# Performance work log

Hardware: AMD Instinct MI355X
Metric: run time of the kernel (lower is better)

The kernel has to match this reference:

```python
import jax, jax.numpy as jnp
import numpy as np

D = 256      # d_v
FF = 512     # ff_dim = max(hidden, d_v)
H = 4        # num_heads
K = 8        # max_set_size
L = 64       # subset universe length
NC = 32768   # n_chains
NB = 4096    # n_batch
EPS = 1e-8   # module eps for masked-mean denom


def setup_inputs() -> dict:
    key = jax.random.key(0)
    ks = jax.random.split(key, 24)
    s = 0.02
    mask = jax.random.randint(ks[2], (NC, L), 0, 2).astype(bool)
    inp = {
        "v": jax.random.normal(ks[0], (NB, L, D), jnp.float32),
        "batch_idx": jax.random.randint(ks[1], (NC,), 0, NB),
        "mask": mask,
        "count": mask.sum(axis=1).astype(jnp.float32),
        "pos_embed": jnp.zeros((1, K, D), jnp.float32),
        "ln1_w": jnp.ones((D,), jnp.float32),
        "ln1_b": jnp.zeros((D,), jnp.float32),
        "in_proj_w": jax.random.normal(ks[3], (3 * D, D), jnp.float32) * s,
        "in_proj_b": jnp.zeros((3 * D,), jnp.float32),
        "out_proj_w": jax.random.normal(ks[4], (D, D), jnp.float32) * s,
        "out_proj_b": jnp.zeros((D,), jnp.float32),
        "ln2_w": jnp.ones((D,), jnp.float32),
        "ln2_b": jnp.zeros((D,), jnp.float32),
        "ff1_w": jax.random.normal(ks[5], (FF, D), jnp.float32) * s,
        "ff1_b": jnp.zeros((FF,), jnp.float32),
        "ff2_w": jax.random.normal(ks[6], (D, FF), jnp.float32) * s,
        "ff2_b": jnp.zeros((D,), jnp.float32),
        "o1_w": jax.random.normal(ks[7], (FF, D + 1), jnp.float32) * s,
        "o1_b": jnp.zeros((FF,), jnp.float32),
        "o2_w": jax.random.normal(ks[8], (D, FF), jnp.float32) * s,
        "o2_b": jnp.zeros((D,), jnp.float32),
    }
    return inp


def _layernorm(x, w, b, eps=1e-5):
    mu = x.mean(-1, keepdims=True)
    var = ((x - mu) ** 2).mean(-1, keepdims=True)
    return (x - mu) * jax.lax.rsqrt(var + eps) * w + b


def reference(v, batch_idx, mask, count, pos_embed, ln1_w, ln1_b, in_proj_w,
              in_proj_b, out_proj_w, out_proj_b, ln2_w, ln2_b, ff1_w, ff1_b,
              ff2_w, ff2_b, o1_w, o1_b, o2_w, o2_b):
    nc, Lm = mask.shape
    # --- topk subset select (index-order packing) ---
    pos = jnp.arange(Lm, dtype=jnp.float32)
    scores = mask.astype(jnp.float32) * (float(Lm) - pos)[None, :]
    top_scores, top_idx = jax.lax.top_k(scores, K)
    picked0 = top_scores > 0
    sortable = jnp.where(picked0, top_idx, Lm)
    sortable = jnp.sort(sortable, axis=1)
    picked = sortable < Lm                       # [NC,K]
    safe_idx = jnp.where(picked, sortable, 0)
    # fused gather: chain_v[c, i] = v[batch_idx[c], i]
    packed = v[batch_idx[:, None], safe_idx]     # [NC,K,D]
    packed = packed * picked[..., None].astype(packed.dtype)
    x = packed + pos_embed[:, :K, :]
    # key padding mask; un-mask position 0 for fully-empty sets
    kpm = ~picked
    empty = jnp.all(kpm, axis=1)
    kpm = kpm.at[:, 0].set(jnp.where(empty, False, kpm[:, 0]))
    # --- one pre-norm transformer encoder layer ---
    h = _layernorm(x, ln1_w, ln1_b)
    qkv = h @ in_proj_w.T + in_proj_b
    q, k_, vv = jnp.split(qkv, 3, axis=-1)
    hd = D // H
    def heads(t):
        return t.reshape(nc, K, H, hd).transpose(0, 2, 1, 3)
    q, k_, vv = heads(q), heads(k_), heads(vv)
    att = jnp.einsum('bhqd,bhkd->bhqk', q, k_) / jnp.sqrt(jnp.float32(hd))
    att = jnp.where(kpm[:, None, None, :], -jnp.inf, att)
    att = jax.nn.softmax(att, axis=-1)
    ao = jnp.einsum('bhqk,bhkd->bhqd', att, vv).transpose(0, 2, 1, 3).reshape(nc, K, D)
    x = x + ao @ out_proj_w.T + out_proj_b
    h2 = _layernorm(x, ln2_w, ln2_b)
    x = x + jax.nn.gelu(h2 @ ff1_w.T + ff1_b, approximate=False) @ ff2_w.T + ff2_b
    # --- masked mean pool ---
    pf = picked.astype(x.dtype)
    denom = jnp.maximum(pf.sum(axis=1, keepdims=True), EPS)
    pooled = (x * pf[..., None]).sum(axis=1) / denom
    pooled = jnp.where(picked.any(axis=1, keepdims=True), pooled, jnp.zeros_like(pooled))
    # --- concat log(1+|S|) and project ---
    feat = jnp.concatenate([pooled, jnp.log1p(count)[:, None]], axis=-1)
    return jax.nn.gelu(feat @ o1_w.T + o1_b, approximate=False) @ o2_w.T + o2_b
```

## Files before the change

### kernel.cpp

```cpp
#include <hip/hip_runtime.h>
#include <hip/hip_bf16.h>
#include <math.h>

typedef short short8 __attribute__((ext_vector_type(8)));
typedef short short4v __attribute__((ext_vector_type(4)));
typedef float f32x4 __attribute__((ext_vector_type(4)));

#define NCC  32768
#define G    4
#define QST  520

#define G1_OFF 0
#define G2_OFF 196608
#define G3_OFF 262144
#define G4_OFF 393216
#define O1_OFF 524288
#define O2_OFF 655360
#define SWZ_SHORTS 786432
#define W256_BYTE_OFF (SWZ_SHORTS * 2)
#define FLAG_BYTE_OFF (W256_BYTE_OFF + 2048)

__device__ __forceinline__ float gelu_f(float x) {
    return x * 0.5f * (1.0f + erff(x * 0.70710678118654752f));
}
__device__ __forceinline__ float bf2f(unsigned short u) {
    union { unsigned int i; float f; } w; w.i = ((unsigned int)u) << 16; return w.f;
}
__device__ __forceinline__ unsigned short f2bf(float f) {
    __hip_bfloat16 h = __float2bfloat16(f);
    return *reinterpret_cast<unsigned short*>(&h);
}
__device__ __forceinline__ int aswz(int row, int scol) {
    return (row * 256 + scol) ^ ((row & 7) << 3);
}
__device__ __forceinline__ int vtswz(int d, int j) {
    return d * 32 + (j ^ ((d & 7) << 2));
}

template<int KTS>
__device__ __forceinline__ void load_bgrp(short8 (&b)[KTS], const unsigned short* __restrict__ base) {
    #pragma unroll
    for (int kt = 0; kt < KTS; kt++)
        b[kt] = *reinterpret_cast<const short8*>(base + (size_t)kt * 512);
}

__global__ void conv_weights(const float* __restrict__ w1, const float* __restrict__ w2,
                             const float* __restrict__ w3, const float* __restrict__ w4,
                             const float* __restrict__ o1, const float* __restrict__ o2,
                             unsigned short* __restrict__ dst, float* __restrict__ w256) {
    int i = blockIdx.x * 256 + threadIdx.x;
    if (i < 98304) {
        const float* src; int kts, sk, base;
        if (i < 24576)      { src = w1; kts = 8;  sk = 256; base = 0; }
        else if (i < 32768) { src = w2; kts = 8;  sk = 256; base = 24576; }
        else if (i < 49152) { src = w3; kts = 8;  sk = 256; base = 32768; }
        else if (i < 65536) { src = w4; kts = 16; sk = 512; base = 49152; }
        else if (i < 81920) { src = o1; kts = 8;  sk = 257; base = 65536; }
        else                { src = o2; kts = 16; sk = 512; base = 81920; }
        int li   = i - base;
        int lane = li & 63;
        int fi   = li >> 6;
        int kt   = fi % kts;
        int nt   = fi / kts;
        int col  = nt * 16 + (lane & 15);
        int k    = kt * 32 + (lane >> 4) * 8;
        const float* s = src + (size_t)col * sk + k;
        unsigned short* d = dst + (size_t)i * 8;
        #pragma unroll
        for (int e = 0; e < 8; e++) d[e] = f2bf(s[e]);
    } else if (i < 98816) {
        int c = i - 98304;
        w256[c] = o1[(size_t)c * 257 + 256];
    }
}

__global__ void detect_mask_fmt(const unsigned int* __restrict__ mw, int nwords, int* __restrict__ flag) {
    __shared__ int s_bad_int, s_bad_float;
    if (threadIdx.x == 0) { s_bad_int = 0; s_bad_float = 0; }
    __syncthreads();
    int bad_int = 0, bad_float = 0;
    for (int i = threadIdx.x; i < nwords; i += blockDim.x) {
        unsigned int w = mw[i];
        if (w > 1u) bad_int = 1;
        if (w != 0u && w != 0x3F800000u) bad_float = 1;
    }
    if (bad_int)   atomicOr(&s_bad_int, 1);
    if (bad_float) atomicOr(&s_bad_float, 1);
    __syncthreads();
    if (threadIdx.x == 0)
        *flag = (!s_bad_int) ? 0 : ((!s_bad_float) ? 2 : 1);
}

__global__ __launch_bounds__(256, 2)
void tsa_main(const float* __restrict__ v,
              const int* __restrict__ batch_idx,
              const void* __restrict__ mask,
              const float* __restrict__ pos_embed,
              const float* __restrict__ ln1_w, const float* __restrict__ ln1_b,
              const float* __restrict__ in_proj_b,
              const float* __restrict__ out_proj_b,
              const float* __restrict__ ln2_w, const float* __restrict__ ln2_b,
              const float* __restrict__ ff1_b, const float* __restrict__ ff2_b,
              const unsigned short* __restrict__ wb,
              const int* __restrict__ mask_flag,
              float* __restrict__ out)
{
    __shared__ unsigned short qkbuf[32 * QST];
    __shared__ unsigned short abuf[32 * 256];
    __shared__ unsigned short attw_s[2][4][16][16];
    __shared__ int s_idx[G][8];
    __shared__ int s_m[G];
    __shared__ int s_bi[G];

    float (*lnred)[32][2] = reinterpret_cast<float (*)[32][2]>(&attw_s[0][0][0][0]);

    const int tid  = threadIdx.x;
    const int lane = tid & 63;
    const int wid  = tid >> 6;
    const int cq   = lane >> 4;
    const int cc   = lane & 15;
    const int cg0  = blockIdx.x * G;
    const int pair = wid >> 1;

    f32x4 xr[2][4];

    {
        int mf = *mask_flag;
        size_t base = (size_t)(cg0 + wid) * 64 + lane;
        int bit;
        if (mf == 0)      bit = ((const int*)mask)[base] != 0;
        else if (mf == 2) bit = ((const float*)mask)[base] != 0.0f;
        else              bit = ((const unsigned char*)mask)[base] != 0;
        unsigned long long bal = __ballot(bit);
        if (lane == 0) {
            int mm = 0; unsigned long long b = bal;
            while (b && mm < 8) { s_idx[wid][mm++] = __ffsll(b) - 1; b &= (b - 1); }
            for (int t = mm; t < 8; t++) s_idx[wid][t] = 0;
            s_m[wid]  = mm;
            s_bi[wid] = batch_idx[cg0 + wid];
        }
    }
    __syncthreads();

    #pragma unroll
    for (int mt = 0; mt < 2; mt++) {
        int c  = 2 * mt + (cq >> 1);
        int m  = s_m[c];
        int bi = s_bi[c];
        #pragma unroll
        for (int rr = 0; rr < 4; rr++) {
            int rowin = (cq & 1) * 4 + rr;
            int vidx  = s_idx[c][rowin];
            #pragma unroll
            for (int nt = 0; nt < 4; nt++) {
                int col  = wid * 64 + nt * 16 + cc;
                float pe = pos_embed[rowin * 256 + col];
                float val = (rowin < m) ? v[((size_t)bi * 64 + vidx) * 256 + col] : 0.0f;
                xr[mt][nt][rr] = val + pe;
            }
        }
    }

    auto do_ln = [&](const float* __restrict__ lw, const float* __restrict__ lb) {
        float sm[2][4], sq[2][4];
        #pragma unroll
        for (int mt = 0; mt < 2; mt++)
            #pragma unroll
            for (int rr = 0; rr < 4; rr++) {
                float s = 0.f, q = 0.f;
                #pragma unroll
                for (int nt = 0; nt < 4; nt++) {
                    float x = xr[mt][nt][rr];
                    s += x; q += x * x;
                }
                sm[mt][rr] = s; sq[mt][rr] = q;
            }
        #pragma unroll
        for (int off = 1; off < 16; off <<= 1) {
            #pragma unroll
            for (int mt = 0; mt < 2; mt++)
                #pragma unroll
                for (int rr = 0; rr < 4; rr++) {
                    sm[mt][rr] += __shfl_xor(sm[mt][rr], off);
                    sq[mt][rr] += __shfl_xor(sq[mt][rr], off);
                }
        }
        __syncthreads();
        if (cc == 0) {
            #pragma unroll
            for (int mt = 0; mt < 2; mt++)
                #pragma unroll
                for (int rr = 0; rr < 4; rr++) {
                    int row = mt * 16 + cq * 4 + rr;
                    lnred[wid][row][0] = sm[mt][rr];
                    lnred[wid][row][1] = sq[mt][rr];
                }
        }
        __syncthreads();
        float mu[2][4], rs[2][4];
        #pragma unroll
        for (int mt = 0; mt < 2; mt++)
            #pragma unroll
            for (int rr = 0; rr < 4; rr++) {
                int row = mt * 16 + cq * 4 + rr;
                float S = 0.f, Q = 0.f;
                #pragma unroll
                for (int w = 0; w < 4; w++) { S += lnred[w][row][0]; Q += lnred[w][row][1]; }
                float m_ = S * (1.0f / 256.0f);
                mu[mt][rr] = m_;
                rs[mt][rr] = rsqrtf(Q * (1.0f / 256.0f) - m_ * m_ + 1e-5f);
            }
        #pragma unroll
        for (int nt = 0; nt < 4; nt++) {
            int col = wid * 64 + nt * 16 + cc;
            float w_ = lw[col], b_ = lb[col];
            #pragma unroll
            for (int mt = 0; mt < 2; mt++)
                #pragma unroll
                for (int rr = 0; rr < 4; rr++) {
                    int row = mt * 16 + cq * 4 + rr;
                    abuf[aswz(row, col)] = f2bf((xr[mt][nt][rr] - mu[mt][rr]) * rs[mt][rr] * w_ + b_);
                }
        }
        __syncthreads();
    };

    auto load_a_from = [&](short8 (&a0)[8], short8 (&a1)[8], const unsigned short* base) {
        #pragma unroll
        for (int kt = 0; kt < 8; kt++) {
            a0[kt] = *reinterpret_cast<const short8*>(&base[aswz(cc,      kt * 32 + cq * 8)]);
            a1[kt] = *reinterpret_cast<const short8*>(&base[aswz(16 + cc, kt * 32 + cq * 8)]);
        }
    };

    do_ln(ln1_w, ln1_b);

    {
        short8 a0[8], a1[8];
        load_a_from(a0, a1, abuf);
        __syncthreads();

        auto bbase = [&](int nt) {
            int gnt = (nt < 8) ? (wid * 8 + nt) : (32 + wid * 4 + (nt - 8));
            return wb + G1_OFF + (size_t)gnt * 8 * 512 + lane * 8;
        };
        short8 bb[2][8];
        load_bgrp<8>(bb[0], bbase(0));
        #pragma unroll
        for (int nt = 0; nt < 12; nt++) {
            if (nt + 1 < 12) load_bgrp<8>(bb[(nt + 1) & 1], bbase(nt + 1));
            float b = (nt < 8) ? in_proj_b[wid * 128 + nt * 16 + cc]
                               : in_proj_b[512 + wid * 64 + (nt - 8) * 16 + cc];
            f32x4 c0 = {b, b, b, b}, c1 = {b, b, b, b};
            #pragma unroll
            for (int kt = 0; kt < 8; kt++) {
                c0 = __builtin_amdgcn_mfma_f32_16x16x32_bf16(a0[kt], bb[nt & 1][kt], c0, 0, 0, 0);
                c1 = __builtin_amdgcn_mfma_f32_16x16x32_bf16(a1[kt], bb[nt & 1][kt], c1, 0, 0, 0);
            }
            if (nt < 8) {
                int col = wid * 128 + nt * 16 + cc;
                #pragma unroll
                for (int r = 0; r < 4; r++) {
                    qkbuf[(cq * 4 + r) * QST + col]      = f2bf(c0[r]);
                    qkbuf[(16 + cq * 4 + r) * QST + col] = f2bf(c1[r]);
                }
            } else {
                int d = wid * 64 + (nt - 8) * 16 + cc;
                short4v p0, p1;
                #pragma unroll
                for (int r = 0; r < 4; r++) { p0[r] = (short)f2bf(c0[r]); p1[r] = (short)f2bf(c1[r]); }
                *reinterpret_cast<short4v*>(&abuf[vtswz(d, cq * 4)])      = p0;
                *reinterpret_cast<short4v*>(&abuf[vtswz(d, 16 + cq * 4)]) = p1;
            }
        }
    }
    __syncthreads();

    {
        #pragma unroll
        for (int hj = 0; hj < 2; hj++) {
            int h = (wid & 1) * 2 + hj;
            f32x4 c = {0.f, 0.f, 0.f, 0.f};
            #pragma unroll
            for (int kt = 0; kt < 2; kt++) {
                short8 qa = *reinterpret_cast<const short8*>(&qkbuf[(pair * 16 + cc) * QST + h * 64 + cq * 8 + kt * 32]);
                short8 kb = *reinterpret_cast<const short8*>(&qkbuf[(pair * 16 + cc) * QST + 256 + h * 64 + cq * 8 + kt * 32]);
                c = __builtin_amdgcn_mfma_f32_16x16x32_bf16(qa, kb, c, 0, 0, 0);
            }
            int jhalf = cc >> 3, jloc = cc & 7;
            #pragma unroll
            for (int r = 0; r < 4; r++) {
                int q = cq * 4 + r;
                int qhalf = q >> 3;
                int m = s_m[pair * 2 + qhalf];
                bool valid = (jhalf == qhalf) && (jloc < m);
                float s = valid ? c[r] * 0.125f : -1e30f;
                float mx = s;
                mx = fmaxf(mx, __shfl_xor(mx, 1));
                mx = fmaxf(mx, __shfl_xor(mx, 2));
                mx = fmaxf(mx, __shfl_xor(mx, 4));
                float e = valid ? __expf(s - mx) : 0.f;
                float se = e;
                se += __shfl_xor(se, 1);
                se += __shfl_xor(se, 2);
                se += __shfl_xor(se, 4);
                attw_s[pair][h][q][cc] = f2bf((se > 0.f) ? e / se : 0.f);
            }
        }
    }
    __syncthreads();

    {
        int jbg = pair * 16 + (cq & 1) * 8;
        #pragma unroll
        for (int hj = 0; hj < 2; hj++) {
            int h = (wid & 1) * 2 + hj;
            short8 pa;
            if (cq < 2) pa = *reinterpret_cast<const short8*>(&attw_s[pair][h][cc][cq * 8]);
            else        pa = (short8)((short)0);
            #pragma unroll
            for (int t = 0; t < 4; t++) {
                int d = h * 64 + t * 16 + cc;
                short4v lo = *reinterpret_cast<const short4v*>(&abuf[vtswz(d, jbg)]);
                short4v hi = *reinterpret_cast<const short4v*>(&abuf[vtswz(d, jbg + 4)]);
                union { short8 v; short4v half2[2]; } u;
                u.half2[0] = lo; u.half2[1] = hi;
                f32x4 c = {0.f, 0.f, 0.f, 0.f};
                c = __builtin_amdgcn_mfma_f32_16x16x32_bf16(pa, u.v, c, 0, 0, 0);
                #pragma unroll
                for (int r = 0; r < 4; r++)
                    qkbuf[aswz(pair * 16 + cq * 4 + r, d)] = f2bf(c[r]);
            }
        }
    }
    __syncthreads();

    {
        short8 a0[8], a1[8];
        load_a_from(a0, a1, qkbuf);
        short8 bb[2][8];
        auto bbase = [&](int nt) {
            return wb + G2_OFF + (size_t)(wid * 4 + nt) * 8 * 512 + lane * 8;
        };
        load_bgrp<8>(bb[0], bbase(0));
        #pragma unroll
        for (int nt = 0; nt < 4; nt++) {
            if (nt + 1 < 4) load_bgrp<8>(bb[(nt + 1) & 1], bbase(nt + 1));
            float b = out_proj_b[wid * 64 + nt * 16 + cc];
            f32x4 c0 = {b, b, b, b}, c1 = {b, b, b, b};
            #pragma unroll
            for (int kt = 0; kt < 8; kt++) {
                c0 = __builtin_amdgcn_mfma_f32_16x16x32_bf16(a0[kt], bb[nt & 1][kt], c0, 0, 0, 0);
                c1 = __builtin_amdgcn_mfma_f32_16x16x32_bf16(a1[kt], bb[nt & 1][kt], c1, 0, 0, 0);
            }
            xr[0][nt] += c0;
            xr[1][nt] += c1;
        }
    }
    __syncthreads();

    do_ln(ln2_w, ln2_b);

    {
        short8 a0[8], a1[8];
        load_a_from(a0, a1, abuf);
        short8 bb[2][8];
        auto bbase = [&](int nt) {
            return wb + G3_OFF + (size_t)(wid * 8 + nt) * 8 * 512 + lane * 8;
        };
        load_bgrp<8>(bb[0], bbase(0));
        #pragma unroll
        for (int nt = 0; nt < 8; nt++) {
            if (nt + 1 < 8) load_bgrp<8>(bb[(nt + 1) & 1], bbase(nt + 1));
            float b = ff1_b[wid * 128 + nt * 16 + cc];
            f32x4 c0 = {b, b, b, b}, c1 = {b, b, b, b};
            #pragma unroll
            for (int kt = 0; kt < 8; kt++) {
                c0 = __builtin_amdgcn_mfma_f32_16x16x32_bf16(a0[kt], bb[nt & 1][kt], c0, 0, 0, 0);
                c1 = __builtin_amdgcn_mfma_f32_16x16x32_bf16(a1[kt], bb[nt & 1][kt], c1, 0, 0, 0);
            }
            int col = wid * 128 + nt * 16 + cc;
            #pragma unroll
            for (int r = 0; r < 4; r++) {
                qkbuf[(cq * 4 + r) * QST + col]      = f2bf(gelu_f(c0[r]));
                qkbuf[(16 + cq * 4 + r) * QST + col] = f2bf(gelu_f(c1[r]));
            }
        }
    }
    __syncthreads();

    {
        f32x4 c[4][2];
        #pragma unroll
        for (int nt = 0; nt < 4; nt++) {
            float b = ff2_b[wid * 64 + nt * 16 + cc];
            c[nt][0] = (f32x4){b, b, b, b};
            c[nt][1] = (f32x4){b, b, b, b};
        }
        #pragma unroll
        for (int half = 0; half < 2; half++) {
            short8 a0[8], a1[8];
            #pragma unroll
            for (int kt = 0; kt < 8; kt++) {
                a0[kt] = *reinterpret_cast<const short8*>(&qkbuf[cc * QST        + half * 256 + kt * 32 + cq * 8]);
                a1[kt] = *reinterpret_cast<const short8*>(&qkbuf[(16 + cc) * QST + half * 256 + kt * 32 + cq * 8]);
            }
            short8 bb[2][8];
            auto bbase = [&](int nt) {
                return wb + G4_OFF + (size_t)((wid * 4 + nt) * 16 + half * 8) * 512 + lane * 8;
            };
            load_bgrp<8>(bb[0], bbase(0));
            #pragma unroll
            for (int nt = 0; nt < 4; nt++) {
                if (nt + 1 < 4) load_bgrp<8>(bb[(nt + 1) & 1], bbase(nt + 1));
                #pragma unroll
                for (int kt = 0; kt < 8; kt++) {
                    c[nt][0] = __builtin_amdgcn_mfma_f32_16x16x32_bf16(a0[kt], bb[nt & 1][kt], c[nt][0], 0, 0, 0);
                    c[nt][1] = __builtin_amdgcn_mfma_f32_16x16x32_bf16(a1[kt], bb[nt & 1][kt], c[nt][1], 0, 0, 0);
                }
            }
        }
        #pragma unroll
        for (int nt = 0; nt < 4; nt++) {
            xr[0][nt] += c[nt][0];
            xr[1][nt] += c[nt][1];
        }
    }

    #pragma unroll
    for (int mt = 0; mt < 2; mt++) {
        int c = 2 * mt + (cq >> 1);
        int m = s_m[c];
        float invm = (m > 0) ? 1.0f / (float)m : 0.0f;
        #pragma unroll
        for (int nt = 0; nt < 4; nt++) {
            float p = 0.f;
            #pragma unroll
            for (int rr = 0; rr < 4; rr++)
                if ((cq & 1) * 4 + rr < m) p += xr[mt][nt][rr];
            p += __shfl_xor(p, 16);
            if ((cq & 1) == 0) {
                int col = wid * 64 + nt * 16 + cc;
                out[(size_t)(cg0 + c) * 256 + col] = p * invm;
            }
        }
    }
}

__global__ __launch_bounds__(256, 2)
void tsa_head(const float* __restrict__ count,
              const float* __restrict__ o1_b, const float* __restrict__ o2_b,
              const unsigned short* __restrict__ wb, const float* __restrict__ w256,
              float* __restrict__ out)
{
    __shared__ unsigned short fbuf[32 * 256];
    __shared__ unsigned short gbuf[32][520];
    __shared__ float cbuf[32];

    const int tid  = threadIdx.x;
    const int lane = tid & 63;
    const int wid  = tid >> 6;
    const int cq   = lane >> 4;
    const int cc   = lane & 15;
    const int c0b  = blockIdx.x * 32;

    for (int i = tid; i < 32 * 256; i += 256) {
        int row = i >> 8, col = i & 255;
        fbuf[aswz(row, col)] = f2bf(out[(size_t)(c0b + row) * 256 + col]);
    }
    if (tid < 32) cbuf[tid] = log1pf(count[c0b + tid]);
    __syncthreads();

    short8 a0[8], a1[8];
    #pragma unroll
    for (int kt = 0; kt < 8; kt++) {
        a0[kt] = *reinterpret_cast<const short8*>(&fbuf[aswz(cc,      kt * 32 + cq * 8)]);
        a1[kt] = *reinterpret_cast<const short8*>(&fbuf[aswz(16 + cc, kt * 32 + cq * 8)]);
    }

    {
        short8 bb[2][8];
        auto bbase = [&](int nt) {
            return wb + O1_OFF + (size_t)(wid * 8 + nt) * 8 * 512 + lane * 8;
        };
        load_bgrp<8>(bb[0], bbase(0));
        #pragma unroll
        for (int nt = 0; nt < 8; nt++) {
            if (nt + 1 < 8) load_bgrp<8>(bb[(nt + 1) & 1], bbase(nt + 1));
            int col  = wid * 128 + nt * 16 + cc;
            float b  = o1_b[col];
            float wc = w256[col];
            f32x4 c0 = {b, b, b, b}, c1 = {b, b, b, b};
            #pragma unroll
            for (int kt = 0; kt < 8; kt++) {
                c0 = __builtin_amdgcn_mfma_f32_16x16x32_bf16(a0[kt], bb[nt & 1][kt], c0, 0, 0, 0);
                c1 = __builtin_amdgcn_mfma_f32_16x16x32_bf16(a1[kt], bb[nt & 1][kt], c1, 0, 0, 0);
            }
            #pragma unroll
            for (int r = 0; r < 4; r++) {
                int r0 = cq * 4 + r, r1 = 16 + cq * 4 + r;
                gbuf[r0][col] = f2bf(gelu_f(c0[r] + cbuf[r0] * wc));
                gbuf[r1][col] = f2bf(gelu_f(c1[r] + cbuf[r1] * wc));
            }
        }
    }
    __syncthreads();

    {
        f32x4 c[4][2];
        #pragma unroll
        for (int nt = 0; nt < 4; nt++) {
            float b = o2_b[wid * 64 + nt * 16 + cc];
            c[nt][0] = (f32x4){b, b, b, b};
            c[nt][1] = (f32x4){b, b, b, b};
        }
        #pragma unroll
        for (int half = 0; half < 2; half++) {
            #pragma unroll
            for (int kt = 0; kt < 8; kt++) {
                a0[kt] = *reinterpret_cast<const short8*>(&gbuf[cc][half * 256 + kt * 32 + cq * 8]);
                a1[kt] = *reinterpret_cast<const short8*>(&gbuf[16 + cc][half * 256 + kt * 32 + cq * 8]);
            }
            short8 bb[2][8];
            auto bbase = [&](int nt) {
                return wb + O2_OFF + (size_t)((wid * 4 + nt) * 16 + half * 8) * 512 + lane * 8;
            };
            load_bgrp<8>(bb[0], bbase(0));
            #pragma unroll
            for (int nt = 0; nt < 4; nt++) {
                if (nt + 1 < 4) load_bgrp<8>(bb[(nt + 1) & 1], bbase(nt + 1));
                #pragma unroll
                for (int kt = 0; kt < 8; kt++) {
                    c[nt][0] = __builtin_amdgcn_mfma_f32_16x16x32_bf16(a0[kt], bb[nt & 1][kt], c[nt][0], 0, 0, 0);
                    c[nt][1] = __builtin_amdgcn_mfma_f32_16x16x32_bf16(a1[kt], bb[nt & 1][kt], c[nt][1], 0, 0, 0);
                }
            }
        }
        #pragma unroll
        for (int nt = 0; nt < 4; nt++) {
            int col = wid * 64 + nt * 16 + cc;
            #pragma unroll
            for (int r = 0; r < 4; r++) {
                out[(size_t)(c0b + cq * 4 + r) * 256 + col]      = c[nt][0][r];
                out[(size_t)(c0b + 16 + cq * 4 + r) * 256 + col] = c[nt][1][r];
            }
        }
    }
}

extern "C" void kernel_launch(void* const* d_in, const int* in_sizes, int n_in,
                              void* d_out, int out_size, void* d_ws, size_t ws_size,
                              hipStream_t stream) {
    const float* v          = (const float*)d_in[0];
    const int*   batch_idx  = (const int*)d_in[1];
    const void*  mask       = d_in[2];
    const float* count      = (const float*)d_in[3];
    const float* pos_embed  = (const float*)d_in[4];
    const float* ln1_w      = (const float*)d_in[5];
    const float* ln1_b      = (const float*)d_in[6];
    const float* in_proj_w  = (const float*)d_in[7];
    const float* in_proj_b  = (const float*)d_in[8];
    const float* out_proj_w = (const float*)d_in[9];
    const float* out_proj_b = (const float*)d_in[10];
    const float* ln2_w      = (const float*)d_in[11];
    const float* ln2_b      = (const float*)d_in[12];
    const float* ff1_w      = (const float*)d_in[13];
    const float* ff1_b      = (const float*)d_in[14];
    const float* ff2_w      = (const float*)d_in[15];
    const float* ff2_b      = (const float*)d_in[16];
    const float* o1_w       = (const float*)d_in[17];
    const float* o1_b       = (const float*)d_in[18];
    const float* o2_w       = (const float*)d_in[19];
    const float* o2_b       = (const float*)d_in[20];
    float* out = (float*)d_out;

    unsigned short* wb = (unsigned short*)d_ws;
    float* w256 = (float*)((char*)d_ws + W256_BYTE_OFF);
    int* flag   = (int*)((char*)d_ws + FLAG_BYTE_OFF);

    conv_weights<<<387, 256, 0, stream>>>(in_proj_w, out_proj_w, ff1_w, ff2_w, o1_w, o2_w, wb, w256);
    detect_mask_fmt<<<1, 256, 0, stream>>>((const unsigned int*)mask, 16384, flag);
    tsa_main<<<NCC / G, 256, 0, stream>>>(v, batch_idx, mask, pos_embed,
                                          ln1_w, ln1_b, in_proj_b, out_proj_b,
                                          ln2_w, ln2_b, ff1_b, ff2_b,
                                          wb, flag, out);
    tsa_head<<<NCC / 32, 256, 0, stream>>>(count, o1_b, o2_b, wb, w256, out);
}
```

Baseline: 613.9 us.

## Swizzle LDS buffers, accumulate residual in MFMA, raise occupancy and MFMA priority

Replaces the padded 520-stride LDS rows for the QK/FF and head buffers with an XOR-swizzled 512-stride layout. This shrinks shared memory so that launch bounds can request three blocks per CU instead of two. The residual adds for out_proj and ff2 now accumulate directly into the xr registers, dropping the separate accumulators and cutting register pressure. It also moves the LayerNorm reduction scratch into qkbuf, drops one barrier, and wraps the MFMA loops in s_setprio. The risks are register spills under the tighter occupancy target and races on the reused lnred scratch.

```diff
diff --git a/kernel.cpp b/kernel.cpp
--- a/kernel.cpp
+++ b/kernel.cpp
@@ -8,7 +8,6 @@
 
 #define NCC  32768
 #define G    4
-#define QST  520
 
 #define G1_OFF 0
 #define G2_OFF 196608
@@ -31,7 +30,10 @@
     return *reinterpret_cast<unsigned short*>(&h);
 }
 __device__ __forceinline__ int aswz(int row, int scol) {
-    return (row * 256 + scol) ^ ((row & 7) << 3);
+    return row * 256 + (scol ^ ((row & 7) << 3));
+}
+__device__ __forceinline__ int qswz(int row, int scol) {
+    return row * 512 + (scol ^ ((row & 7) << 3));
 }
 __device__ __forceinline__ int vtswz(int d, int j) {
     return d * 32 + (j ^ ((d & 7) << 2));
@@ -91,7 +93,7 @@
         *flag = (!s_bad_int) ? 0 : ((!s_bad_float) ? 2 : 1);
 }
 
-__global__ __launch_bounds__(256, 2)
+__global__ __launch_bounds__(256, 3)
 void tsa_main(const float* __restrict__ v,
               const int* __restrict__ batch_idx,
               const void* __restrict__ mask,
@@ -105,14 +107,14 @@
               const int* __restrict__ mask_flag,
               float* __restrict__ out)
 {
-    __shared__ unsigned short qkbuf[32 * QST];
+    __shared__ unsigned short qkbuf[32 * 512];
     __shared__ unsigned short abuf[32 * 256];
     __shared__ unsigned short attw_s[2][4][16][16];
     __shared__ int s_idx[G][8];
     __shared__ int s_m[G];
     __shared__ int s_bi[G];
 
-    float (*lnred)[32][2] = reinterpret_cast<float (*)[32][2]>(&attw_s[0][0][0][0]);
+    float* lnred = reinterpret_cast<float*>(qkbuf);
 
     const int tid  = threadIdx.x;
     const int lane = tid & 63;
@@ -185,15 +187,14 @@
                     sq[mt][rr] += __shfl_xor(sq[mt][rr], off);
                 }
         }
-        __syncthreads();
         if (cc == 0) {
             #pragma unroll
             for (int mt = 0; mt < 2; mt++)
                 #pragma unroll
                 for (int rr = 0; rr < 4; rr++) {
                     int row = mt * 16 + cq * 4 + rr;
-                    lnred[wid][row][0] = sm[mt][rr];
-                    lnred[wid][row][1] = sq[mt][rr];
+                    lnred[(wid * 32 + row) * 2 + 0] = sm[mt][rr];
+                    lnred[(wid * 32 + row) * 2 + 1] = sq[mt][rr];
                 }
         }
         __syncthreads();
@@ -205,7 +206,10 @@
                 int row = mt * 16 + cq * 4 + rr;
                 float S = 0.f, Q = 0.f;
                 #pragma unroll
-                for (int w = 0; w < 4; w++) { S += lnred[w][row][0]; Q += lnred[w][row][1]; }
+                for (int w = 0; w < 4; w++) {
+                    S += lnred[(w * 32 + row) * 2 + 0];
+                    Q += lnred[(w * 32 + row) * 2 + 1];
+                }
                 float m_ = S * (1.0f / 256.0f);
                 mu[mt][rr] = m_;
                 rs[mt][rr] = rsqrtf(Q * (1.0f / 256.0f) - m_ * m_ + 1e-5f);
@@ -225,19 +229,26 @@
         __syncthreads();
     };
 
-    auto load_a_from = [&](short8 (&a0)[8], short8 (&a1)[8], const unsigned short* base) {
+    auto load_a_abuf = [&](short8 (&a0)[8], short8 (&a1)[8]) {
         #pragma unroll
         for (int kt = 0; kt < 8; kt++) {
-            a0[kt] = *reinterpret_cast<const short8*>(&base[aswz(cc,      kt * 32 + cq * 8)]);
-            a1[kt] = *reinterpret_cast<const short8*>(&base[aswz(16 + cc, kt * 32 + cq * 8)]);
+            a0[kt] = *reinterpret_cast<const short8*>(&abuf[aswz(cc,      kt * 32 + cq * 8)]);
+            a1[kt] = *reinterpret_cast<const short8*>(&abuf[aswz(16 + cc, kt * 32 + cq * 8)]);
         }
     };
+    auto load_a_qk = [&](short8 (&a0)[8], short8 (&a1)[8], int so) {
+        #pragma unroll
+        for (int kt = 0; kt < 8; kt++) {
+            a0[kt] = *reinterpret_cast<const short8*>(&qkbuf[qswz(cc,      so + kt * 32 + cq * 8)]);
+            a1[kt] = *reinterpret_cast<const short8*>(&qkbuf[qswz(16 + cc, so + kt * 32 + cq * 8)]);
+        }
+    };
 
     do_ln(ln1_w, ln1_b);
 
     {
         short8 a0[8], a1[8];
-        load_a_from(a0, a1, abuf);
+        load_a_abuf(a0, a1);
         __syncthreads();
 
         auto bbase = [&](int nt) {
@@ -252,17 +263,19 @@
             float b = (nt < 8) ? in_proj_b[wid * 128 + nt * 16 + cc]
                                : in_proj_b[512 + wid * 64 + (nt - 8) * 16 + cc];
             f32x4 c0 = {b, b, b, b}, c1 = {b, b, b, b};
+            __builtin_amdgcn_s_setprio(1);
             #pragma unroll
             for (int kt = 0; kt < 8; kt++) {
                 c0 = __builtin_amdgcn_mfma_f32_16x16x32_bf16(a0[kt], bb[nt & 1][kt], c0, 0, 0, 0);
                 c1 = __builtin_amdgcn_mfma_f32_16x16x32_bf16(a1[kt], bb[nt & 1][kt], c1, 0, 0, 0);
             }
+            __builtin_amdgcn_s_setprio(0);
             if (nt < 8) {
                 int col = wid * 128 + nt * 16 + cc;
                 #pragma unroll
                 for (int r = 0; r < 4; r++) {
-                    qkbuf[(cq * 4 + r) * QST + col]      = f2bf(c0[r]);
-                    qkbuf[(16 + cq * 4 + r) * QST + col] = f2bf(c1[r]);
+                    qkbuf[qswz(cq * 4 + r, col)]      = f2bf(c0[r]);
+                    qkbuf[qswz(16 + cq * 4 + r, col)] = f2bf(c1[r]);
                 }
             } else {
                 int d = wid * 64 + (nt - 8) * 16 + cc;
@@ -283,8 +296,8 @@
             f32x4 c = {0.f, 0.f, 0.f, 0.f};
             #pragma unroll
             for (int kt = 0; kt < 2; kt++) {
-                short8 qa = *reinterpret_cast<const short8*>(&qkbuf[(pair * 16 + cc) * QST + h * 64 + cq * 8 + kt * 32]);
-                short8 kb = *reinterpret_cast<const short8*>(&qkbuf[(pair * 16 + cc) * QST + 256 + h * 64 + cq * 8 + kt * 32]);
+                short8 qa = *reinterpret_cast<const short8*>(&qkbuf[qswz(pair * 16 + cc, h * 64 + cq * 8 + kt * 32)]);
+                short8 kb = *reinterpret_cast<const short8*>(&qkbuf[qswz(pair * 16 + cc, 256 + h * 64 + cq * 8 + kt * 32)]);
                 c = __builtin_amdgcn_mfma_f32_16x16x32_bf16(qa, kb, c, 0, 0, 0);
             }
             int jhalf = cc >> 3, jloc = cc & 7;
@@ -329,7 +342,7 @@
                 c = __builtin_amdgcn_mfma_f32_16x16x32_bf16(pa, u.v, c, 0, 0, 0);
                 #pragma unroll
                 for (int r = 0; r < 4; r++)
-                    qkbuf[aswz(pair * 16 + cq * 4 + r, d)] = f2bf(c[r]);
+                    qkbuf[qswz(pair * 16 + cq * 4 + r, d)] = f2bf(c[r]);
             }
         }
     }
@@ -337,7 +350,7 @@
 
     {
         short8 a0[8], a1[8];
-        load_a_from(a0, a1, qkbuf);
+        load_a_qk(a0, a1, 0);
         short8 bb[2][8];
         auto bbase = [&](int nt) {
             return wb + G2_OFF + (size_t)(wid * 4 + nt) * 8 * 512 + lane * 8;
@@ -347,14 +360,15 @@
         for (int nt = 0; nt < 4; nt++) {
             if (nt + 1 < 4) load_bgrp<8>(bb[(nt + 1) & 1], bbase(nt + 1));
             float b = out_proj_b[wid * 64 + nt * 16 + cc];
-            f32x4 c0 = {b, b, b, b}, c1 = {b, b, b, b};
+            #pragma unroll
+            for (int r = 0; r < 4; r++) { xr[0][nt][r] += b; xr[1][nt][r] += b; }
+            __builtin_amdgcn_s_setprio(1);
             #pragma unroll
             for (int kt = 0; kt < 8; kt++) {
-                c0 = __builtin_amdgcn_mfma_f32_16x16x32_bf16(a0[kt], bb[nt & 1][kt], c0, 0, 0, 0);
-                c1 = __builtin_amdgcn_mfma_f32_16x16x32_bf16(a1[kt], bb[nt & 1][kt], c1, 0, 0, 0);
-            }
-            xr[0][nt] += c0;
-            xr[1][nt] += c1;
+                xr[0][nt] = __builtin_amdgcn_mfma_f32_16x16x32_bf16(a0[kt], bb[nt & 1][kt], xr[0][nt], 0, 0, 0);
+                xr[1][nt] = __builtin_amdgcn_mfma_f32_16x16x32_bf16(a1[kt], bb[nt & 1][kt], xr[1][nt], 0, 0, 0);
+            }
+            __builtin_amdgcn_s_setprio(0);
         }
     }
     __syncthreads();
@@ -363,7 +377,7 @@
 
     {
         short8 a0[8], a1[8];
-        load_a_from(a0, a1, abuf);
+        load_a_abuf(a0, a1);
         short8 bb[2][8];
         auto bbase = [&](int nt) {
             return wb + G3_OFF + (size_t)(wid * 8 + nt) * 8 * 512 + lane * 8;
@@ -374,37 +388,34 @@
             if (nt + 1 < 8) load_bgrp<8>(bb[(nt + 1) & 1], bbase(nt + 1));
             float b = ff1_b[wid * 128 + nt * 16 + cc];
             f32x4 c0 = {b, b, b, b}, c1 = {b, b, b, b};
+            __builtin_amdgcn_s_setprio(1);
             #pragma unroll
             for (int kt = 0; kt < 8; kt++) {
                 c0 = __builtin_amdgcn_mfma_f32_16x16x32_bf16(a0[kt], bb[nt & 1][kt], c0, 0, 0, 0);
                 c1 = __builtin_amdgcn_mfma_f32_16x16x32_bf16(a1[kt], bb[nt & 1][kt], c1, 0, 0, 0);
             }
+            __builtin_amdgcn_s_setprio(0);
             int col = wid * 128 + nt * 16 + cc;
             #pragma unroll
             for (int r = 0; r < 4; r++) {
-                qkbuf[(cq * 4 + r) * QST + col]      = f2bf(gelu_f(c0[r]));
-                qkbuf[(16 + cq * 4 + r) * QST + col] = f2bf(gelu_f(c1[r]));
-            }
-        }
-    }
-    __syncthreads();
-
-    {
-        f32x4 c[4][2];
+                qkbuf[qswz(cq * 4 + r, col)]      = f2bf(gelu_f(c0[r]));
+                qkbuf[qswz(16 + cq * 4 + r, col)] = f2bf(gelu_f(c1[r]));
+            }
+        }
+    }
+    __syncthreads();
+
+    {
         #pragma unroll
         for (int nt = 0; nt < 4; nt++) {
             float b = ff2_b[wid * 64 + nt * 16 + cc];
-            c[nt][0] = (f32x4){b, b, b, b};
-            c[nt][1] = (f32x4){b, b, b, b};
+            #pragma unroll
+            for (int r = 0; r < 4; r++) { xr[0][nt][r] += b; xr[1][nt][r] += b; }
         }
         #pragma unroll
         for (int half = 0; half < 2; half++) {
             short8 a0[8], a1[8];
-            #pragma unroll
-            for (int kt = 0; kt < 8; kt++) {
-                a0[kt] = *reinterpret_cast<const short8*>(&qkbuf[cc * QST        + half * 256 + kt * 32 + cq * 8]);
-                a1[kt] = *reinterpret_cast<const short8*>(&qkbuf[(16 + cc) * QST + half * 256 + kt * 32 + cq * 8]);
-            }
+            load_a_qk(a0, a1, half * 256);
             short8 bb[2][8];
             auto bbase = [&](int nt) {
                 return wb + G4_OFF + (size_t)((wid * 4 + nt) * 16 + half * 8) * 512 + lane * 8;
@@ -413,17 +424,14 @@
             #pragma unroll
             for (int nt = 0; nt < 4; nt++) {
                 if (nt + 1 < 4) load_bgrp<8>(bb[(nt + 1) & 1], bbase(nt + 1));
+                __builtin_amdgcn_s_setprio(1);
                 #pragma unroll
                 for (int kt = 0; kt < 8; kt++) {
-                    c[nt][0] = __builtin_amdgcn_mfma_f32_16x16x32_bf16(a0[kt], bb[nt & 1][kt], c[nt][0], 0, 0, 0);
-                    c[nt][1] = __builtin_amdgcn_mfma_f32_16x16x32_bf16(a1[kt], bb[nt & 1][kt], c[nt][1], 0, 0, 0);
-                }
-            }
-        }
-        #pragma unroll
-        for (int nt = 0; nt < 4; nt++) {
-            xr[0][nt] += c[nt][0];
-            xr[1][nt] += c[nt][1];
+                    xr[0][nt] = __builtin_amdgcn_mfma_f32_16x16x32_bf16(a0[kt], bb[nt & 1][kt], xr[0][nt], 0, 0, 0);
+                    xr[1][nt] = __builtin_amdgcn_mfma_f32_16x16x32_bf16(a1[kt], bb[nt & 1][kt], xr[1][nt], 0, 0, 0);
+                }
+                __builtin_amdgcn_s_setprio(0);
+            }
         }
     }
 
@@ -447,14 +455,14 @@
     }
 }
 
-__global__ __launch_bounds__(256, 2)
+__global__ __launch_bounds__(256, 3)
 void tsa_head(const float* __restrict__ count,
               const float* __restrict__ o1_b, const float* __restrict__ o2_b,
               const unsigned short* __restrict__ wb, const float* __restrict__ w256,
               float* __restrict__ out)
 {
     __shared__ unsigned short fbuf[32 * 256];
-    __shared__ unsigned short gbuf[32][520];
+    __shared__ unsigned short gbuf[32 * 512];
     __shared__ float cbuf[32];
 
     const int tid  = threadIdx.x;
@@ -491,16 +499,18 @@
             float b  = o1_b[col];
             float wc = w256[col];
             f32x4 c0 = {b, b, b, b}, c1 = {b, b, b, b};
+            __builtin_amdgcn_s_setprio(1);
             #pragma unroll
             for (int kt = 0; kt < 8; kt++) {
                 c0 = __builtin_amdgcn_mfma_f32_16x16x32_bf16(a0[kt], bb[nt & 1][kt], c0, 0, 0, 0);
                 c1 = __builtin_amdgcn_mfma_f32_16x16x32_bf16(a1[kt], bb[nt & 1][kt], c1, 0, 0, 0);
             }
+            __builtin_amdgcn_s_setprio(0);
             #pragma unroll
             for (int r = 0; r < 4; r++) {
                 int r0 = cq * 4 + r, r1 = 16 + cq * 4 + r;
-                gbuf[r0][col] = f2bf(gelu_f(c0[r] + cbuf[r0] * wc));
-                gbuf[r1][col] = f2bf(gelu_f(c1[r] + cbuf[r1] * wc));
+                gbuf[qswz(r0, col)] = f2bf(gelu_f(c0[r] + cbuf[r0] * wc));
+                gbuf[qswz(r1, col)] = f2bf(gelu_f(c1[r] + cbuf[r1] * wc));
             }
         }
     }
@@ -518,8 +528,8 @@
         for (int half = 0; half < 2; half++) {
             #pragma unroll
             for (int kt = 0; kt < 8; kt++) {
-                a0[kt] = *reinterpret_cast<const short8*>(&gbuf[cc][half * 256 + kt * 32 + cq * 8]);
-                a1[kt] = *reinterpret_cast<const short8*>(&gbuf[16 + cc][half * 256 + kt * 32 + cq * 8]);
+                a0[kt] = *reinterpret_cast<const short8*>(&gbuf[qswz(cc,      half * 256 + kt * 32 + cq * 8)]);
+                a1[kt] = *reinterpret_cast<const short8*>(&gbuf[qswz(16 + cc, half * 256 + kt * 32 + cq * 8)]);
             }
             short8 bb[2][8];
             auto bbase = [&](int nt) {
@@ -529,11 +539,13 @@
             #pragma unroll
             for (int nt = 0; nt < 4; nt++) {
                 if (nt + 1 < 4) load_bgrp<8>(bb[(nt + 1) & 1], bbase(nt + 1));
+                __builtin_amdgcn_s_setprio(1);
                 #pragma unroll
                 for (int kt = 0; kt < 8; kt++) {
                     c[nt][0] = __builtin_amdgcn_mfma_f32_16x16x32_bf16(a0[kt], bb[nt & 1][kt], c[nt][0], 0, 0, 0);
                     c[nt][1] = __builtin_amdgcn_mfma_f32_16x16x32_bf16(a1[kt], bb[nt & 1][kt], c[nt][1], 0, 0, 0);
                 }
+                __builtin_amdgcn_s_setprio(0);
             }
         }
         #pragma unroll
```

New measurement: 1.363 ms. +122.1%, slower.
